# Optimization experiments

Hardware: AMD Instinct MI355X
Metric: run time of the kernel (lower is better)

Reference implementation:

```python
import jax, jax.numpy as jnp
import numpy as np
from jax import lax

WINS = [3, 5, 7, 11, 15, 19]
MAXW = 19
PAD = MAXW // 2 + 1          # 10, matches F.pad(..., max_wh//2+1)
NEG_HALF = (-MAXW) // 2      # -10, matches torch's `-self.max_wh // 2` (floor div)
EPS_IN = 1e-5
EPS_DEV = 1e-6


def _conv(x, w, b, dil):
    # x: [B,C,H,W], w: [O,I,kh,kw], 'same' padding with dilation
    y = lax.conv_general_dilated(x, w, (1, 1), 'SAME',
                                 rhs_dilation=(dil, dil),
                                 dimension_numbers=('NCHW', 'OIHW', 'NCHW'))
    return y + b[None, :, None, None]


def _inorm_relu(y):
    # InstanceNorm2d(affine=False): per-sample per-channel over H,W, biased var
    m = jnp.mean(y, axis=(2, 3), keepdims=True)
    v = jnp.mean((y - m) ** 2, axis=(2, 3), keepdims=True)
    return jax.nn.relu((y - m) * lax.rsqrt(v + EPS_IN))


def _integral(x):
    # x: [B,H,W,C] -> padded double cumsum (integral image) [B,H+2P,W+2P,C]
    xp = jnp.pad(x, ((0, 0), (PAD, PAD), (PAD, PAD), (0, 0)))
    return jnp.cumsum(jnp.cumsum(xp, axis=1), axis=2)


def _box_sum(ii, h, w):
    # 4-corner integral-image lookup; slices reproduce torch offsets exactly
    top = MAXW // 2 - h // 2
    bot = top + h
    left = MAXW // 2 - w // 2
    right = left + w
    top0 = NEG_HALF - h // 2 - 1
    bot0 = top0 + h
    left0 = NEG_HALF - w // 2 - 1
    right0 = left0 + w
    return (ii[:, top:top0, left:left0] + ii[:, bot:bot0, right:right0]
            - ii[:, top:top0, right:right0] - ii[:, bot:bot0, left:left0])


def _multi_window_mean(x):
    # x: [B,H,W,1] -> [B,n_wins,H,W,1] of window means
    ii = _integral(x)
    cnt_ii = _integral(jnp.ones_like(x[:1]))  # [1,...] pixel-count integral
    means = [_box_sum(ii, hw, hw) / _box_sum(cnt_ii, hw, hw) for hw in WINS]
    return jnp.stack(means, axis=1)


def _sauvola(x1, k, R):
    E_x = _multi_window_mean(x1)
    E_x2 = _multi_window_mean(x1 * x1)
    dev = jnp.sqrt(jnp.maximum(E_x2 - E_x ** 2, EPS_DEV))
    return E_x * (1.0 + k * (dev / R - 1.0))  # [B,n,H,W,1]


def setup_inputs() -> dict:
    key = jax.random.key(0)
    ks = jax.random.split(key, 16)
    B, H, W = 4, 768, 768
    base = 4
    chans = [1, 4, 8, 12, 16, 20, 24]
    d = {'x': jax.random.uniform(ks[0], (B, 1, H, W), dtype=jnp.float32)}
    names = ['conv1', 'convs1', 'convs2', 'convs3', 'convs4', 'convs5']
    for i, nm in enumerate(names):
        cin, cout = chans[i], chans[i + 1]
        d[nm + '_w'] = jax.random.normal(ks[1 + i], (cout, cin, 3, 3), dtype=jnp.float32) * 0.1
        d[nm + '_b'] = jax.random.normal(ks[7 + i], (cout,), dtype=jnp.float32) * 0.01
    d['conv2_w'] = jax.random.normal(ks[13], (len(WINS), 24, 3, 3), dtype=jnp.float32) * 0.1
    d['conv2_b'] = jax.random.normal(ks[14], (len(WINS),), dtype=jnp.float32) * 0.01
    d['k'] = jnp.full((1, len(WINS), 1, 1, 1), 0.2, dtype=jnp.float32)
    d['R'] = jnp.full((1, len(WINS), 1, 1, 1), 0.5, dtype=jnp.float32)
    d['alpha'] = jnp.full((1, 1, 1, 1), 16.0, dtype=jnp.float32)
    return d


def reference(x, conv1_w, conv1_b, convs1_w, convs1_b, convs2_w, convs2_b,
              convs3_w, convs3_b, convs4_w, convs4_b, convs5_w, convs5_b,
              conv2_w, conv2_b, k, R, alpha):
    y = _inorm_relu(_conv(x, conv1_w, conv1_b, 1))
    for w, b in ((convs1_w, convs1_b), (convs2_w, convs2_b), (convs3_w, convs3_b),
                 (convs4_w, convs4_b), (convs5_w, convs5_b)):
        y = _inorm_relu(_conv(y, w, b, 2))
    f = jax.nn.softmax(_conv(y, conv2_w, conv2_b, 1), axis=1)  # [B,n,H,W]
    x1 = jnp.transpose(x, (0, 2, 3, 1))                        # [B,H,W,1]
    th = _sauvola(x1, k, R)                                    # [B,n,H,W,1]
    th1 = jnp.sum(f[..., None] * th, axis=1)                   # [B,H,W,1]
    diff = (x1 - th1) * alpha / (1.0 - 0.0)                    # img_range (0,1)
    return jnp.transpose(diff, (0, 3, 1, 2))                   # [B,1,H,W]
```

## Files before the change

### kernel.cpp

```cpp
#include <hip/hip_runtime.h>
#include <math.h>

#define BDIM 256
#define BDIM2 512
typedef __bf16 bf16;
typedef __bf16 bf16x4 __attribute__((ext_vector_type(4)));
typedef __bf16 bf16x8 __attribute__((ext_vector_type(8)));
typedef float f32x4 __attribute__((ext_vector_type(4)));
typedef float f32x2 __attribute__((ext_vector_type(2)));

template <bool V> struct BC { static constexpr bool value = V; };

constexpr int B_ = 4, H_ = 768, W_ = 768;
constexpr int HW_ = H_ * W_;
constexpr int TS = 16;
constexpr int NTB = W_ / TS;
constexpr int NBLK = HW_ / (TS * TS);
constexpr int TS2 = 32;
constexpr int NTB2 = W_ / TS2;
constexpr int NBLK2 = HW_ / (TS2 * TS2);

constexpr int PMAX_FLOATS = 4 * NBLK * 48;
constexpr int OUT_ELEMS   = B_ * HW_;

__device__ void repack_one(const float* __restrict__ src, bf16* __restrict__ dst,
                           int CIN, int CINP, int COUT, int NT16, int KPP)
{
    const int n_ = NT16 * KPP;
    for (int idx = threadIdx.x; idx < n_; idx += BDIM) {
        const int n = idx / KPP, k = idx - n * KPP;
        const int tap = k / CINP, ci = k - tap * CINP;
        float v = 0.f;
        if (n < COUT && tap < 9 && ci < CIN)
            v = src[(n * CIN + ci) * 9 + tap];
        dst[idx] = (bf16)v;
    }
}

__global__ __launch_bounds__(BDIM) void repack_all(
    const float* w0, const float* w1, const float* w2, const float* w3,
    const float* w4, const float* w5, const float* wf,
    bf16* r0, bf16* r1, bf16* r2, bf16* r3, bf16* r4, bf16* r5, bf16* rf)
{
    switch (blockIdx.x) {
        case 0: repack_one(w0, r0, 1,  8,  4,  16, 104); break;
        case 1: repack_one(w1, r1, 4,  8,  8,  16, 104); break;
        case 2: repack_one(w2, r2, 8,  8,  12, 16, 104); break;
        case 3: repack_one(w3, r3, 12, 16, 16, 16, 168); break;
        case 4: repack_one(w4, r4, 16, 16, 20, 32, 168); break;
        case 5: repack_one(w5, r5, 20, 24, 24, 32, 232); break;
        case 6: repack_one(wf, rf, 24, 24, 6,  16, 232); break;
    }
}

template <int CIN, int CINP, int COUT, int DIL, bool FIRST>
__global__ __launch_bounds__(BDIM) void conv_mfma(
    const void* __restrict__ inv,
    const float* __restrict__ prevStats,
    const bf16* __restrict__ wp,
    const float* __restrict__ bias,
    bf16* __restrict__ y,
    float* __restrict__ partials,
    int NBT)
{
    constexpr int TW = TS + 2 * DIL;
    constexpr int KP = ((9 * CINP + 31) / 32) * 32;
    constexpr int KPP = KP + 8;
    constexpr int NT = (COUT + 15) / 16;
    constexpr int KS = KP / 32;
    constexpr int CSTR = (CINP == 16) ? 24 : CINP;
    __shared__ __align__(16) bf16 tile[TW * TW * CSTR];
    __shared__ float sred[4][2 * COUT];

    const int s = blockIdx.x / NBLK;
    const int blk = blockIdx.x - s * NBLK;
    const int ti = blk / NTB, tj = blk - ti * NTB;
    const int i0 = ti * TS - DIL, j0 = tj * TS - DIL;
    const int t = threadIdx.x;
    const bool interior = (i0 >= 0) & (j0 >= 0) &
                          (i0 + TW <= H_) & (j0 + TW <= W_);

    const float* ps = prevStats + s * 2 * CIN;
    auto stage = [&](auto bc) {
        constexpr bool IN = decltype(bc)::value;
        for (int loc = t; loc < TW * TW; loc += BDIM) {
            const int rr = loc / TW, cc = loc - rr * TW;
            const int gi = i0 + rr, gj = j0 + cc;
            bool ok = true;
            if constexpr (!IN)
                ok = (gi >= 0) & (gi < H_) & (gj >= 0) & (gj < W_);
            float lv[CSTR];
#pragma unroll
            for (int c = 0; c < CSTR; ++c) lv[c] = 0.f;
            if (ok) {
                if constexpr (FIRST) {
                    const float* xg = (const float*)inv + (size_t)s * HW_;
                    lv[0] = xg[(size_t)gi * W_ + gj];
                } else {
                    const bf16* ing = (const bf16*)inv +
                                      ((size_t)s * HW_ + (size_t)gi * W_ + gj) * CIN;
                    if constexpr (CIN % 8 == 0) {
#pragma unroll
                        for (int qq = 0; qq < CIN / 8; ++qq) {
                            bf16x8 raw = ((const bf16x8*)ing)[qq];
#pragma unroll
                            for (int u = 0; u < 8; ++u) {
                                const int ci = 8 * qq + u;
                                lv[ci] = fmaxf(fmaf((float)raw[u], ps[2 * ci], ps[2 * ci + 1]), 0.f);
                            }
                        }
                    } else {
#pragma unroll
                        for (int qq = 0; qq < CIN / 4; ++qq) {
                            bf16x4 raw = ((const bf16x4*)ing)[qq];
#pragma unroll
                            for (int u = 0; u < 4; ++u) {
                                const int ci = 4 * qq + u;
                                lv[ci] = fmaxf(fmaf((float)raw[u], ps[2 * ci], ps[2 * ci + 1]), 0.f);
                            }
                        }
                    }
                }
            }
            bf16* lp = tile + loc * CSTR;
#pragma unroll
            for (int g = 0; g < CSTR / 8; ++g) {
                bf16x8 pk;
#pragma unroll
                for (int u = 0; u < 8; ++u) pk[u] = (bf16)lv[8 * g + u];
                *(bf16x8*)(lp + 8 * g) = pk;
            }
        }
    };
    if (interior) stage(BC<true>{}); else stage(BC<false>{});
    __syncthreads();

    const int wave = t >> 6, lane = t & 63, q = lane >> 4, ln = lane & 15;
    f32x4 acc[4][NT];
#pragma unroll
    for (int mt = 0; mt < 4; ++mt)
#pragma unroll
        for (int u = 0; u < NT; ++u) acc[mt][u] = (f32x4){0.f, 0.f, 0.f, 0.f};

    auto aOff = [&](int ks) -> int {
        int k0 = ks * 32 + q * 8;
        int tap = k0 / CINP;
        int ci0 = k0 - tap * CINP;
        if (tap > 8) { tap = 0; ci0 = 0; }
        const int ky = tap / 3, kx = tap - 3 * ky;
        return (ky * DIL * TW + kx * DIL) * CSTR + ci0;
    };

    bf16x8 bfr[NT], bfrN[NT];
    bf16x8 af[4], afN[4];
#pragma unroll
    for (int u = 0; u < NT; ++u)
        bfr[u] = *(const bf16x8*)&wp[(u * 16 + ln) * KPP + q * 8];
    {
        const int ao = aOff(0);
#pragma unroll
        for (int mt = 0; mt < 4; ++mt)
            af[mt] = *(const bf16x8*)&tile[((wave * 4 + mt) * TW + ln) * CSTR + ao];
    }

#pragma unroll
    for (int ks = 0; ks < KS; ++ks) {
        if (ks + 1 < KS) {
#pragma unroll
            for (int u = 0; u < NT; ++u)
                bfrN[u] = *(const bf16x8*)&wp[(u * 16 + ln) * KPP + (ks + 1) * 32 + q * 8];
            const int ao = aOff(ks + 1);
#pragma unroll
            for (int mt = 0; mt < 4; ++mt)
                afN[mt] = *(const bf16x8*)&tile[((wave * 4 + mt) * TW + ln) * CSTR + ao];
        }
#pragma unroll
        for (int mt = 0; mt < 4; ++mt)
#pragma unroll
            for (int u = 0; u < NT; ++u)
                acc[mt][u] = __builtin_amdgcn_mfma_f32_16x16x32_bf16(
                    af[mt], bfr[u], acc[mt][u], 0, 0, 0);
#pragma unroll
        for (int u = 0; u < NT; ++u) bfr[u] = bfrN[u];
#pragma unroll
        for (int mt = 0; mt < 4; ++mt) af[mt] = afN[mt];
    }

#pragma unroll
    for (int u = 0; u < NT; ++u) {
        const int n = u * 16 + ln;
        const float bv = (n < COUT) ? bias[n] : 0.f;
        float s1 = 0.f, s2 = 0.f;
#pragma unroll
        for (int mt = 0; mt < 4; ++mt)
#pragma unroll
            for (int r = 0; r < 4; ++r) {
                const float v = acc[mt][u][r] + bv;
                acc[mt][u][r] = v;
                s1 += v; s2 += v * v;
            }
        s1 += __shfl_xor(s1, 16); s1 += __shfl_xor(s1, 32);
        s2 += __shfl_xor(s2, 16); s2 += __shfl_xor(s2, 32);
        if (lane < 16 && n < COUT) { sred[wave][n] = s1; sred[wave][COUT + n] = s2; }
    }
    __syncthreads();
    if (t < 2 * COUT) {
        partials[(size_t)t * NBT + (size_t)s * NBLK + blk] =
            sred[0][t] + sred[1][t] + sred[2][t] + sred[3][t];
    }

    bf16* ost = tile;
#pragma unroll
    for (int u = 0; u < NT; ++u) {
        const int n = u * 16 + ln;
        if (n < COUT) {
#pragma unroll
            for (int mt = 0; mt < 4; ++mt)
#pragma unroll
                for (int r = 0; r < 4; ++r) {
                    const int pl = (wave * 4 + mt) * 16 + q * 4 + r;
                    ost[pl * COUT + n] = (bf16)acc[mt][u][r];
                }
        }
    }
    __syncthreads();

    const int lr = t >> 4, lc = t & 15;
    bf16* yp = y + (size_t)s * HW_ * COUT +
               ((size_t)(ti * TS + lr) * W_ + (tj * TS + lc)) * COUT;
    const bf16* sp = ost + t * COUT;
    if constexpr (COUT % 8 == 0) {
#pragma unroll
        for (int g = 0; g < COUT / 8; ++g)
            ((bf16x8*)yp)[g] = ((const bf16x8*)sp)[g];
    } else {
#pragma unroll
        for (int g = 0; g < COUT / 4; ++g)
            ((bf16x4*)yp)[g] = ((const bf16x4*)sp)[g];
    }
}

template <int COUT>
__global__ __launch_bounds__(BDIM) void reduce_stats(
    const float* __restrict__ partials, float* __restrict__ stats, int NBT)
{
    const int s = blockIdx.x / COUT;
    const int co = blockIdx.x - s * COUT;
    const float* P1 = partials + (size_t)co * NBT + (size_t)s * NBLK;
    const float* P2 = partials + (size_t)(COUT + co) * NBT + (size_t)s * NBLK;
    float s1 = 0.f, s2 = 0.f;
    for (int k = threadIdx.x; k < NBLK; k += BDIM) {
        s1 += P1[k];
        s2 += P2[k];
    }
#pragma unroll
    for (int off = 32; off; off >>= 1) {
        s1 += __shfl_xor(s1, off);
        s2 += __shfl_xor(s2, off);
    }
    __shared__ float l1[4], l2[4];
    const int lane = threadIdx.x & 63, wave = threadIdx.x >> 6;
    if (lane == 0) { l1[wave] = s1; l2[wave] = s2; }
    __syncthreads();
    if (threadIdx.x == 0) {
        float t1 = l1[0] + l1[1] + l1[2] + l1[3];
        float t2 = l2[0] + l2[1] + l2[2] + l2[3];
        float m = t1 / (float)HW_;
        float var = t2 / (float)HW_ - m * m;
        const float rs = rsqrtf(var + 1e-5f);
        stats[((size_t)s * COUT + co) * 2 + 0] = rs;
        stats[((size_t)s * COUT + co) * 2 + 1] = -m * rs;
    }
}

__global__ __launch_bounds__(BDIM2) void conv2_sauvola(
    const bf16* __restrict__ in, const float* __restrict__ prevStats,
    const bf16* __restrict__ wp, const float* __restrict__ bias,
    const float* __restrict__ x,
    const float* __restrict__ kArr, const float* __restrict__ RArr,
    const float* __restrict__ alphaP, float* __restrict__ outp)
{
    constexpr int CIN = 24, CINP = 24, COUT = 6;
    constexpr int TW = TS2 + 2;
    constexpr int KPP = 232, KS = 7, CSTR = 24;
    constexpr int R9 = 9;
    constexpr int TSW = TS2 + 2 * R9;
    constexpr int ISTR = 51;
    constexpr int SLOG_STR = 7;
    __shared__ __align__(16) bf16 tile[TW * TW * CSTR];
    __shared__ __align__(16) f32x2 I12[(TSW + 1) * ISTR];

    const int s = blockIdx.x / NBLK2;
    const int blk = blockIdx.x - s * NBLK2;
    const int ti = blk / NTB2, tj = blk - ti * NTB2;
    const int i0 = ti * TS2 - 1, j0 = tj * TS2 - 1;
    const int is0 = ti * TS2 - R9, js0 = tj * TS2 - R9;
    const int t = threadIdx.x;
    const float* xs = x + (size_t)s * HW_;
    const bool interior = (is0 >= 0) & (js0 >= 0) &
                          (is0 + TSW <= H_) & (js0 + TSW <= W_);

    const float* ps = prevStats + s * 2 * CIN;
    auto stage = [&](auto bc) {
        constexpr bool IN = decltype(bc)::value;
        for (int loc = t; loc < TW * TW; loc += BDIM2) {
            const int rr = loc / TW, cc = loc - rr * TW;
            const int gi = i0 + rr, gj = j0 + cc;
            bool ok = true;
            if constexpr (!IN)
                ok = (gi >= 0) & (gi < H_) & (gj >= 0) & (gj < W_);
            float lv[CSTR];
#pragma unroll
            for (int c = 0; c < CSTR; ++c) lv[c] = 0.f;
            if (ok) {
                const bf16* ing = in + ((size_t)s * HW_ + (size_t)gi * W_ + gj) * CIN;
#pragma unroll
                for (int qq = 0; qq < CIN / 8; ++qq) {
                    bf16x8 raw = ((const bf16x8*)ing)[qq];
#pragma unroll
                    for (int u = 0; u < 8; ++u) {
                        const int ci = 8 * qq + u;
                        lv[ci] = fmaxf(fmaf((float)raw[u], ps[2 * ci], ps[2 * ci + 1]), 0.f);
                    }
                }
            }
            bf16* lp = tile + loc * CSTR;
#pragma unroll
            for (int g = 0; g < CSTR / 8; ++g) {
                bf16x8 pk;
#pragma unroll
                for (int u = 0; u < 8; ++u) pk[u] = (bf16)lv[8 * g + u];
                *(bf16x8*)(lp + 8 * g) = pk;
            }
        }
        for (int loc = t; loc < TSW * TSW; loc += BDIM2) {
            const int rr = loc / TSW, cc = loc - rr * TSW;
            const int gi = is0 + rr, gj = js0 + cc;
            float v;
            if constexpr (IN) {
                v = xs[(size_t)gi * W_ + gj];
            } else {
                v = 0.f;
                if ((gi >= 0) & (gi < H_) & (gj >= 0) & (gj < W_))
                    v = xs[(size_t)gi * W_ + gj];
            }
            I12[(rr + 1) * ISTR + cc + 1] = (f32x2){v, v * v};
        }
    };
    if (interior) stage(BC<true>{}); else stage(BC<false>{});
    for (int idx = t; idx < (TSW + 1) + TSW; idx += BDIM2) {
        if (idx < TSW + 1) I12[idx] = (f32x2){0.f, 0.f};
        else I12[(idx - (TSW + 1) + 1) * ISTR] = (f32x2){0.f, 0.f};
    }
    __syncthreads();

    const int wave = t >> 6, lane = t & 63, q = lane >> 4, ln = lane & 15;
    f32x4 acc[8];
#pragma unroll
    for (int mt = 0; mt < 8; ++mt) acc[mt] = (f32x4){0.f, 0.f, 0.f, 0.f};

    auto aOff = [&](int ks) -> int {
        int k0 = ks * 32 + q * 8;
        int tap = k0 / CINP;
        int ci0 = k0 - tap * CINP;
        if (tap > 8) { tap = 0; ci0 = 0; }
        const int ky = tap / 3, kx = tap - 3 * ky;
        return (ky * TW + kx) * CSTR + ci0;
    };

#pragma unroll
    for (int ks = 0; ks < KS; ++ks) {
        const bf16x8 bfr = *(const bf16x8*)&wp[ln * KPP + ks * 32 + q * 8];
        const int ao = aOff(ks);
#pragma unroll
        for (int mt = 0; mt < 8; ++mt) {
            const int Mt = wave * 8 + mt;
            const bf16x8 af = *(const bf16x8*)
                &tile[(((Mt >> 1)) * TW + (Mt & 1) * 16 + ln) * CSTR + ao];
            acc[mt] = __builtin_amdgcn_mfma_f32_16x16x32_bf16(af, bfr, acc[mt], 0, 0, 0);
        }
    }
    __syncthreads();

    float* slog = (float*)tile;
    const float bv = (ln < COUT) ? bias[ln] : 0.f;
#pragma unroll
    for (int mt = 0; mt < 8; ++mt)
#pragma unroll
        for (int r = 0; r < 4; ++r)
            if (ln < COUT) {
                const int pl = (wave * 8 + mt) * 16 + q * 4 + r;
                slog[pl * SLOG_STR + ln] = acc[mt][r] + bv;
            }
    if (t < TSW) {
        f32x2* row = I12 + (t + 1) * ISTR;
        f32x2 a = (f32x2){0.f, 0.f};
#pragma unroll 2
        for (int c = 1; c <= TSW; ++c) { a += row[c]; row[c] = a; }
    }
    __syncthreads();

    if (t < TSW) {
        const int c = t + 1;
        f32x2 a = (f32x2){0.f, 0.f};
#pragma unroll 2
        for (int r = 1; r <= TSW; ++r) {
            f32x2* p = &I12[r * ISTR + c];
            a += *p; *p = a;
        }
    }
    float e0[COUT], e1[COUT];
    auto softmax_of = [&](int p, float* e) {
        float mx = slog[p * SLOG_STR];
#pragma unroll
        for (int co = 1; co < COUT; ++co) mx = fmaxf(mx, slog[p * SLOG_STR + co]);
        float sm = 0.f;
#pragma unroll
        for (int co = 0; co < COUT; ++co) { e[co] = __expf(slog[p * SLOG_STR + co] - mx); sm += e[co]; }
        const float inv = 1.f / sm;
#pragma unroll
        for (int co = 0; co < COUT; ++co) e[co] *= inv;
    };
    softmax_of(t, e0);
    softmax_of(t + BDIM2, e1);
    float c0w[6], c1w[6];
#pragma unroll
    for (int wi = 0; wi < 6; ++wi) {
        const float kk = kArr[wi], rr = RArr[wi];
        c0w[wi] = kk / rr;
        c1w[wi] = 1.f - kk;
    }
    const int pr0 = t >> 5, pc0 = t & 31;
    const int pr1 = pr0 + 16, pc1 = pc0;
    const int gi0 = ti * TS2 + pr0, gj0 = tj * TS2 + pc0;
    const int gi1 = ti * TS2 + pr1, gj1 = tj * TS2 + pc1;
    const float xv0 = xs[(size_t)gi0 * W_ + gj0];
    const float xv1 = xs[(size_t)gi1 * W_ + gj1];
    const float alpha = alphaP[0];
    __syncthreads();

    const int wins[6] = {3, 5, 7, 11, 15, 19};
    const float invc_tab[6] = {1.f / 9.f,  1.f / 25.f,  1.f / 49.f,
                               1.f / 121.f, 1.f / 225.f, 1.f / 361.f};
    auto sauv = [&](int pr, int pc, int gi, int gj, const float* e) -> float {
        float th1 = 0.f;
        if (interior) {
#pragma unroll
            for (int wi = 0; wi < 6; ++wi) {
                const int r = wins[wi] >> 1;
                const float invc = invc_tab[wi];
                const int top = pr + R9 - r, bot = pr + R9 + r + 1;
                const int lef = pc + R9 - r, rig = pc + R9 + r + 1;
                const f32x2 Atl = I12[top * ISTR + lef];
                const f32x2 Atr = I12[top * ISTR + rig];
                const f32x2 Abl = I12[bot * ISTR + lef];
                const f32x2 Abr = I12[bot * ISTR + rig];
                const f32x2 sm2 = Abr - Atr - Abl + Atl;
                const float Ex = sm2.x * invc;
                const float Ex2 = sm2.y * invc;
                const float dev = sqrtf(fmaxf(Ex2 - Ex * Ex, 1e-6f));
                const float th = Ex * fmaf(dev, c0w[wi], c1w[wi]);
                th1 = fmaf(e[wi], th, th1);
            }
        } else {
#pragma unroll
            for (int wi = 0; wi < 6; ++wi) {
                const int r = wins[wi] >> 1;
                const int r0 = max(gi - r, 0), r1i = min(gi + r, H_ - 1);
                const int c0 = max(gj - r, 0), c1 = min(gj + r, W_ - 1);
                const float invc = 1.f / (float)((r1i - r0 + 1) * (c1 - c0 + 1));
                const int top = pr + R9 - r, bot = pr + R9 + r + 1;
                const int lef = pc + R9 - r, rig = pc + R9 + r + 1;
                const f32x2 Atl = I12[top * ISTR + lef];
                const f32x2 Atr = I12[top * ISTR + rig];
                const f32x2 Abl = I12[bot * ISTR + lef];
                const f32x2 Abr = I12[bot * ISTR + rig];
                const f32x2 sm2 = Abr - Atr - Abl + Atl;
                const float Ex = sm2.x * invc;
                const float Ex2 = sm2.y * invc;
                const float dev = sqrtf(fmaxf(Ex2 - Ex * Ex, 1e-6f));
                const float th = Ex * fmaf(dev, c0w[wi], c1w[wi]);
                th1 = fmaf(e[wi], th, th1);
            }
        }
        return th1;
    };
    const float th10 = sauv(pr0, pc0, gi0, gj0, e0);
    const float th11 = sauv(pr1, pc1, gi1, gj1, e1);
    outp[(size_t)s * HW_ + (size_t)gi0 * W_ + gj0] = (xv0 - th10) * alpha;
    outp[(size_t)s * HW_ + (size_t)gi1 * W_ + gj1] = (xv1 - th11) * alpha;
}

extern "C" void kernel_launch(void* const* d_in, const int* in_sizes, int n_in,
                              void* d_out, int out_size, void* d_ws, size_t ws_size,
                              hipStream_t stream) {
    const float* x   = (const float*)d_in[0];
    const float* w0  = (const float*)d_in[1];  const float* b0 = (const float*)d_in[2];
    const float* w1  = (const float*)d_in[3];  const float* b1 = (const float*)d_in[4];
    const float* w2  = (const float*)d_in[5];  const float* b2 = (const float*)d_in[6];
    const float* w3  = (const float*)d_in[7];  const float* b3 = (const float*)d_in[8];
    const float* w4  = (const float*)d_in[9];  const float* b4 = (const float*)d_in[10];
    const float* w5  = (const float*)d_in[11]; const float* b5 = (const float*)d_in[12];
    const float* wf  = (const float*)d_in[13]; const float* bf = (const float*)d_in[14];
    const float* kA  = (const float*)d_in[15];
    const float* RA  = (const float*)d_in[16];
    const float* alp = (const float*)d_in[17];
    float* out = (float*)d_out;
    (void)n_in; (void)in_sizes; (void)out_size;

    float* partials = out + (OUT_ELEMS - PMAX_FLOATS - 256);
    float* stats    = out + (OUT_ELEMS - 224);

    auto need = [](int nb) -> size_t {
        size_t o = 0;
        auto al = [&](size_t bytes) { o += (bytes + 255) & ~(size_t)255; };
        al((size_t)nb * HW_ * 20 * 2);
        al((size_t)nb * HW_ * 24 * 2);
        al(1664 * 2); al(1664 * 2); al(1664 * 2); al(2688 * 2);
        al(5376 * 2); al(7424 * 2); al(3712 * 2);
        return o;
    };
    int nb = 1;
    if (ws_size >= need(4)) nb = 4;
    else if (ws_size >= need(2)) nb = 2;

    char* ws = (char*)d_ws;
    size_t off = 0;
    auto alloc = [&](size_t bytes) -> void* {
        void* p = ws + off;
        off += (bytes + 255) & ~(size_t)255;
        return p;
    };
    bf16*  bufA = (bf16*)alloc((size_t)nb * HW_ * 20 * 2);
    bf16*  bufB = (bf16*)alloc((size_t)nb * HW_ * 24 * 2);
    bf16* r0 = (bf16*)alloc(1664 * 2);
    bf16* r1 = (bf16*)alloc(1664 * 2);
    bf16* r2 = (bf16*)alloc(1664 * 2);
    bf16* r3 = (bf16*)alloc(2688 * 2);
    bf16* r4 = (bf16*)alloc(5376 * 2);
    bf16* r5 = (bf16*)alloc(7424 * 2);
    bf16* rf = (bf16*)alloc(3712 * 2);

    const dim3 blk(BDIM);
    const int cg = nb * NBLK;
    const int NBT = nb * NBLK;

    repack_all<<<7, blk, 0, stream>>>(w0, w1, w2, w3, w4, w5, wf,
                                      r0, r1, r2, r3, r4, r5, rf);

    for (int it = 0; it < B_ / nb; ++it) {
        const float* xc   = x   + (size_t)it * nb * HW_;
        float*       outc = out + (size_t)it * nb * HW_;

        conv_mfma<1, 8, 4, 1, true><<<cg, blk, 0, stream>>>(xc, nullptr, r0, b0, bufA, partials, NBT);
        reduce_stats<4><<<nb * 4, blk, 0, stream>>>(partials, stats, NBT);

        conv_mfma<4, 8, 8, 2, false><<<cg, blk, 0, stream>>>(bufA, stats, r1, b1, bufB, partials, NBT);
        reduce_stats<8><<<nb * 8, blk, 0, stream>>>(partials, stats, NBT);

        conv_mfma<8, 8, 12, 2, false><<<cg, blk, 0, stream>>>(bufB, stats, r2, b2, bufA, partials, NBT);
        reduce_stats<12><<<nb * 12, blk, 0, stream>>>(partials, stats, NBT);

        conv_mfma<12, 16, 16, 2, false><<<cg, blk, 0, stream>>>(bufA, stats, r3, b3, bufB, partials, NBT);
        reduce_stats<16><<<nb * 16, blk, 0, stream>>>(partials, stats, NBT);

        conv_mfma<16, 16, 20, 2, false><<<cg, blk, 0, stream>>>(bufB, stats, r4, b4, bufA, partials, NBT);
        reduce_stats<20><<<nb * 20, blk, 0, stream>>>(partials, stats, NBT);

        conv_mfma<20, 24, 24, 2, false><<<cg, blk, 0, stream>>>(bufA, stats, r5, b5, bufB, partials, NBT);
        reduce_stats<24><<<nb * 24, blk, 0, stream>>>(partials, stats, NBT);

        conv2_sauvola<<<nb * NBLK2, dim3(BDIM2), 0, stream>>>(
            bufB, stats, rf, bf, xc, kA, RA, alp, outc);
    }
}
```

Before: 404.6 us.

## Replace per-layer stats reduction kernels with atomics and enlarge conv tiles

```diff
diff --git a/kernel.cpp b/kernel.cpp
--- a/kernel.cpp
+++ b/kernel.cpp
@@ -13,15 +13,13 @@
 
 constexpr int B_ = 4, H_ = 768, W_ = 768;
 constexpr int HW_ = H_ * W_;
-constexpr int TS = 16;
-constexpr int NTB = W_ / TS;
-constexpr int NBLK = HW_ / (TS * TS);
 constexpr int TS2 = 32;
 constexpr int NTB2 = W_ / TS2;
 constexpr int NBLK2 = HW_ / (TS2 * TS2);
 
-constexpr int PMAX_FLOATS = 4 * NBLK * 48;
-constexpr int OUT_ELEMS   = B_ * HW_;
+constexpr int ACC_SLOT_FLOATS = 4 * 48 * 16;
+constexpr int ACC_SLOTS = 24;
+constexpr int ACC_FLOATS = ACC_SLOTS * ACC_SLOT_FLOATS;
 
 __device__ void repack_one(const float* __restrict__ src, bf16* __restrict__ dst,
                            int CIN, int CINP, int COUT, int NT16, int KPP)
@@ -40,7 +38,8 @@
 __global__ __launch_bounds__(BDIM) void repack_all(
     const float* w0, const float* w1, const float* w2, const float* w3,
     const float* w4, const float* w5, const float* wf,
-    bf16* r0, bf16* r1, bf16* r2, bf16* r3, bf16* r4, bf16* r5, bf16* rf)
+    bf16* r0, bf16* r1, bf16* r2, bf16* r3, bf16* r4, bf16* r5, bf16* rf,
+    float* acc)
 {
     switch (blockIdx.x) {
         case 0: repack_one(w0, r0, 1,  8,  4,  16, 104); break;
@@ -50,40 +49,58 @@
         case 4: repack_one(w4, r4, 16, 16, 20, 32, 168); break;
         case 5: repack_one(w5, r5, 20, 24, 24, 32, 232); break;
         case 6: repack_one(wf, rf, 24, 24, 6,  16, 232); break;
+        case 7:
+            for (int idx = threadIdx.x; idx < ACC_FLOATS; idx += BDIM)
+                acc[idx] = 0.f;
+            break;
     }
 }
 
 template <int CIN, int CINP, int COUT, int DIL, bool FIRST>
-__global__ __launch_bounds__(BDIM) void conv_mfma(
+__global__ __launch_bounds__(BDIM2) void conv_mfma(
     const void* __restrict__ inv,
-    const float* __restrict__ prevStats,
+    const float* __restrict__ accPrev,
     const bf16* __restrict__ wp,
     const float* __restrict__ bias,
     bf16* __restrict__ y,
-    float* __restrict__ partials,
-    int NBT)
+    float* __restrict__ accOut)
 {
-    constexpr int TW = TS + 2 * DIL;
+    constexpr int TW = TS2 + 2 * DIL;
     constexpr int KP = ((9 * CINP + 31) / 32) * 32;
     constexpr int KPP = KP + 8;
     constexpr int NT = (COUT + 15) / 16;
     constexpr int KS = KP / 32;
     constexpr int CSTR = (CINP == 16) ? 24 : CINP;
-    __shared__ __align__(16) bf16 tile[TW * TW * CSTR];
-    __shared__ float sred[4][2 * COUT];
-
-    const int s = blockIdx.x / NBLK;
-    const int blk = blockIdx.x - s * NBLK;
-    const int ti = blk / NTB, tj = blk - ti * NTB;
-    const int i0 = ti * TS - DIL, j0 = tj * TS - DIL;
+    constexpr int SMEM = (TW * TW * CSTR > TS2 * TS2 * COUT)
+                             ? TW * TW * CSTR : TS2 * TS2 * COUT;
+    __shared__ __align__(16) bf16 tile[SMEM];
+    __shared__ float sred[8][2 * COUT];
+    __shared__ float psl[2 * CIN];
+
+    const int s = blockIdx.x / NBLK2;
+    const int blk = blockIdx.x - s * NBLK2;
+    const int ti = blk / NTB2, tj = blk - ti * NTB2;
+    const int i0 = ti * TS2 - DIL, j0 = tj * TS2 - DIL;
     const int t = threadIdx.x;
     const bool interior = (i0 >= 0) & (j0 >= 0) &
                           (i0 + TW <= H_) & (j0 + TW <= W_);
 
-    const float* ps = prevStats + s * 2 * CIN;
+    if constexpr (!FIRST) {
+        if (t < CIN) {
+            const float t1 = accPrev[((size_t)s * 48 + t) * 16];
+            const float t2 = accPrev[((size_t)s * 48 + CIN + t) * 16];
+            const float m = t1 / (float)HW_;
+            const float var = t2 / (float)HW_ - m * m;
+            const float rs = rsqrtf(var + 1e-5f);
+            psl[2 * t] = rs;
+            psl[2 * t + 1] = -m * rs;
+        }
+        __syncthreads();
+    }
+
     auto stage = [&](auto bc) {
         constexpr bool IN = decltype(bc)::value;
-        for (int loc = t; loc < TW * TW; loc += BDIM) {
+        for (int loc = t; loc < TW * TW; loc += BDIM2) {
             const int rr = loc / TW, cc = loc - rr * TW;
             const int gi = i0 + rr, gj = j0 + cc;
             bool ok = true;
@@ -106,7 +123,7 @@
 #pragma unroll
                             for (int u = 0; u < 8; ++u) {
                                 const int ci = 8 * qq + u;
-                                lv[ci] = fmaxf(fmaf((float)raw[u], ps[2 * ci], ps[2 * ci + 1]), 0.f);
+                                lv[ci] = fmaxf(fmaf((float)raw[u], psl[2 * ci], psl[2 * ci + 1]), 0.f);
                             }
                         }
                     } else {
@@ -116,7 +133,7 @@
 #pragma unroll
                             for (int u = 0; u < 4; ++u) {
                                 const int ci = 4 * qq + u;
-                                lv[ci] = fmaxf(fmaf((float)raw[u], ps[2 * ci], ps[2 * ci + 1]), 0.f);
+                                lv[ci] = fmaxf(fmaf((float)raw[u], psl[2 * ci], psl[2 * ci + 1]), 0.f);
                             }
                         }
                     }
@@ -136,9 +153,9 @@
     __syncthreads();
 
     const int wave = t >> 6, lane = t & 63, q = lane >> 4, ln = lane & 15;
-    f32x4 acc[4][NT];
-#pragma unroll
-    for (int mt = 0; mt < 4; ++mt)
+    f32x4 acc[8][NT];
+#pragma unroll
+    for (int mt = 0; mt < 8; ++mt)
 #pragma unroll
         for (int u = 0; u < NT; ++u) acc[mt][u] = (f32x4){0.f, 0.f, 0.f, 0.f};
 
@@ -151,39 +168,23 @@
         return (ky * DIL * TW + kx * DIL) * CSTR + ci0;
     };
 
-    bf16x8 bfr[NT], bfrN[NT];
-    bf16x8 af[4], afN[4];
-#pragma unroll
-    for (int u = 0; u < NT; ++u)
-        bfr[u] = *(const bf16x8*)&wp[(u * 16 + ln) * KPP + q * 8];
-    {
-        const int ao = aOff(0);
-#pragma unroll
-        for (int mt = 0; mt < 4; ++mt)
-            af[mt] = *(const bf16x8*)&tile[((wave * 4 + mt) * TW + ln) * CSTR + ao];
-    }
-
 #pragma unroll
     for (int ks = 0; ks < KS; ++ks) {
-        if (ks + 1 < KS) {
-#pragma unroll
-            for (int u = 0; u < NT; ++u)
-                bfrN[u] = *(const bf16x8*)&wp[(u * 16 + ln) * KPP + (ks + 1) * 32 + q * 8];
-            const int ao = aOff(ks + 1);
-#pragma unroll
-            for (int mt = 0; mt < 4; ++mt)
-                afN[mt] = *(const bf16x8*)&tile[((wave * 4 + mt) * TW + ln) * CSTR + ao];
-        }
-#pragma unroll
-        for (int mt = 0; mt < 4; ++mt)
+        bf16x8 bfr[NT];
+#pragma unroll
+        for (int u = 0; u < NT; ++u)
+            bfr[u] = *(const bf16x8*)&wp[(u * 16 + ln) * KPP + ks * 32 + q * 8];
+        const int ao = aOff(ks);
+#pragma unroll
+        for (int mt = 0; mt < 8; ++mt) {
+            const int Mt = wave * 8 + mt;
+            const bf16x8 af = *(const bf16x8*)
+                &tile[(((Mt >> 1)) * TW + (Mt & 1) * 16 + ln) * CSTR + ao];
 #pragma unroll
             for (int u = 0; u < NT; ++u)
                 acc[mt][u] = __builtin_amdgcn_mfma_f32_16x16x32_bf16(
-                    af[mt], bfr[u], acc[mt][u], 0, 0, 0);
-#pragma unroll
-        for (int u = 0; u < NT; ++u) bfr[u] = bfrN[u];
-#pragma unroll
-        for (int mt = 0; mt < 4; ++mt) af[mt] = afN[mt];
+                    af, bfr[u], acc[mt][u], 0, 0, 0);
+        }
     }
 
 #pragma unroll
@@ -192,7 +193,7 @@
         const float bv = (n < COUT) ? bias[n] : 0.f;
         float s1 = 0.f, s2 = 0.f;
 #pragma unroll
-        for (int mt = 0; mt < 4; ++mt)
+        for (int mt = 0; mt < 8; ++mt)
 #pragma unroll
             for (int r = 0; r < 4; ++r) {
                 const float v = acc[mt][u][r] + bv;
@@ -205,8 +206,10 @@
     }
     __syncthreads();
     if (t < 2 * COUT) {
-        partials[(size_t)t * NBT + (size_t)s * NBLK + blk] =
-            sred[0][t] + sred[1][t] + sred[2][t] + sred[3][t];
+        float v = 0.f;
+#pragma unroll
+        for (int w = 0; w < 8; ++w) v += sred[w][t];
+        atomicAdd(&accOut[((size_t)s * 48 + t) * 16], v);
     }
 
     bf16* ost = tile;
@@ -215,66 +218,35 @@
         const int n = u * 16 + ln;
         if (n < COUT) {
 #pragma unroll
-            for (int mt = 0; mt < 4; ++mt)
+            for (int mt = 0; mt < 8; ++mt)
 #pragma unroll
                 for (int r = 0; r < 4; ++r) {
-                    const int pl = (wave * 4 + mt) * 16 + q * 4 + r;
+                    const int pl = (wave * 8 + mt) * 16 + q * 4 + r;
                     ost[pl * COUT + n] = (bf16)acc[mt][u][r];
                 }
         }
     }
     __syncthreads();
 
-    const int lr = t >> 4, lc = t & 15;
-    bf16* yp = y + (size_t)s * HW_ * COUT +
-               ((size_t)(ti * TS + lr) * W_ + (tj * TS + lc)) * COUT;
-    const bf16* sp = ost + t * COUT;
-    if constexpr (COUT % 8 == 0) {
-#pragma unroll
-        for (int g = 0; g < COUT / 8; ++g)
-            ((bf16x8*)yp)[g] = ((const bf16x8*)sp)[g];
-    } else {
-#pragma unroll
-        for (int g = 0; g < COUT / 4; ++g)
-            ((bf16x4*)yp)[g] = ((const bf16x4*)sp)[g];
+    for (int p = t; p < TS2 * TS2; p += BDIM2) {
+        const int lr = p >> 5, lc = p & 31;
+        bf16* yp = y + (size_t)s * HW_ * COUT +
+                   ((size_t)(ti * TS2 + lr) * W_ + (tj * TS2 + lc)) * COUT;
+        const bf16* sp = ost + p * COUT;
+        if constexpr (COUT % 8 == 0) {
+#pragma unroll
+            for (int g = 0; g < COUT / 8; ++g)
+                ((bf16x8*)yp)[g] = ((const bf16x8*)sp)[g];
+        } else {
+#pragma unroll
+            for (int g = 0; g < COUT / 4; ++g)
+                ((bf16x4*)yp)[g] = ((const bf16x4*)sp)[g];
+        }
     }
 }
 
-template <int COUT>
-__global__ __launch_bounds__(BDIM) void reduce_stats(
-    const float* __restrict__ partials, float* __restrict__ stats, int NBT)
-{
-    const int s = blockIdx.x / COUT;
-    const int co = blockIdx.x - s * COUT;
-    const float* P1 = partials + (size_t)co * NBT + (size_t)s * NBLK;
-    const float* P2 = partials + (size_t)(COUT + co) * NBT + (size_t)s * NBLK;
-    float s1 = 0.f, s2 = 0.f;
-    for (int k = threadIdx.x; k < NBLK; k += BDIM) {
-        s1 += P1[k];
-        s2 += P2[k];
-    }
-#pragma unroll
-    for (int off = 32; off; off >>= 1) {
-        s1 += __shfl_xor(s1, off);
-        s2 += __shfl_xor(s2, off);
-    }
-    __shared__ float l1[4], l2[4];
-    const int lane = threadIdx.x & 63, wave = threadIdx.x >> 6;
-    if (lane == 0) { l1[wave] = s1; l2[wave] = s2; }
-    __syncthreads();
-    if (threadIdx.x == 0) {
-        float t1 = l1[0] + l1[1] + l1[2] + l1[3];
-        float t2 = l2[0] + l2[1] + l2[2] + l2[3];
-        float m = t1 / (float)HW_;
-        float var = t2 / (float)HW_ - m * m;
-        const float rs = rsqrtf(var + 1e-5f);
-        stats[((size_t)s * COUT + co) * 2 + 0] = rs;
-        stats[((size_t)s * COUT + co) * 2 + 1] = -m * rs;
-    }
-}
-
 __global__ __launch_bounds__(BDIM2) void conv2_sauvola(
-    const bf16* __restrict__ in, const float* __restrict__ prevStats,
+    const bf16* __restrict__ in, const float* __restrict__ accPrev,
     const bf16* __restrict__ wp, const float* __restrict__ bias,
     const float* __restrict__ x,
     const float* __restrict__ kArr, const float* __restrict__ RArr,
@@ -289,6 +261,7 @@
     constexpr int SLOG_STR = 7;
     __shared__ __align__(16) bf16 tile[TW * TW * CSTR];
     __shared__ __align__(16) f32x2 I12[(TSW + 1) * ISTR];
+    __shared__ float psl[2 * CIN];
 
     const int s = blockIdx.x / NBLK2;
     const int blk = blockIdx.x - s * NBLK2;
@@ -300,7 +273,17 @@
     const bool interior = (is0 >= 0) & (js0 >= 0) &
                           (is0 + TSW <= H_) & (js0 + TSW <= W_);
 
-    const float* ps = prevStats + s * 2 * CIN;
+    if (t < CIN) {
+        const float t1 = accPrev[((size_t)s * 48 + t) * 16];
+        const float t2 = accPrev[((size_t)s * 48 + CIN + t) * 16];
+        const float m = t1 / (float)HW_;
+        const float var = t2 / (float)HW_ - m * m;
+        const float rs = rsqrtf(var + 1e-5f);
+        psl[2 * t] = rs;
+        psl[2 * t + 1] = -m * rs;
+    }
+    __syncthreads();
+
     auto stage = [&](auto bc) {
         constexpr bool IN = decltype(bc)::value;
         for (int loc = t; loc < TW * TW; loc += BDIM2) {
@@ -320,7 +303,7 @@
 #pragma unroll
                     for (int u = 0; u < 8; ++u) {
                         const int ci = 8 * qq + u;
-                        lv[ci] = fmaxf(fmaf((float)raw[u], ps[2 * ci], ps[2 * ci + 1]), 0.f);
+                        lv[ci] = fmaxf(fmaf((float)raw[u], psl[2 * ci], psl[2 * ci + 1]), 0.f);
                     }
                 }
             }
@@ -508,9 +491,6 @@
     float* out = (float*)d_out;
     (void)n_in; (void)in_sizes; (void)out_size;
 
-    float* partials = out + (OUT_ELEMS - PMAX_FLOATS - 256);
-    float* stats    = out + (OUT_ELEMS - 224);
-
     auto need = [](int nb) -> size_t {
         size_t o = 0;
         auto al = [&](size_t bytes) { o += (bytes + 255) & ~(size_t)255; };
@@ -518,6 +498,7 @@
         al((size_t)nb * HW_ * 24 * 2);
         al(1664 * 2); al(1664 * 2); al(1664 * 2); al(2688 * 2);
         al(5376 * 2); al(7424 * 2); al(3712 * 2);
+        al((size_t)ACC_FLOATS * 4);
         return o;
     };
     int nb = 1;
@@ -540,37 +521,32 @@
     bf16* r4 = (bf16*)alloc(5376 * 2);
     bf16* r5 = (bf16*)alloc(7424 * 2);
     bf16* rf = (bf16*)alloc(3712 * 2);
-
-    const dim3 blk(BDIM);
-    const int cg = nb * NBLK;
-    const int NBT = nb * NBLK;
-
-    repack_all<<<7, blk, 0, stream>>>(w0, w1, w2, w3, w4, w5, wf,
-                                      r0, r1, r2, r3, r4, r5, rf);
+    float* acc = (float*)alloc((size_t)ACC_FLOATS * 4);
+
+    const int cg = nb * NBLK2;
+
+    repack_all<<<8, dim3(BDIM), 0, stream>>>(w0, w1, w2, w3, w4, w5, wf,
+                                             r0, r1, r2, r3, r4, r5, rf, acc);
 
     for (int it = 0; it < B_ / nb; ++it) {
         const float* xc   = x   + (size_t)it * nb * HW_;
         float*       outc = out + (size_t)it * nb * HW_;
-
-        conv_mfma<1, 8, 4, 1, true><<<cg, blk, 0, stream>>>(xc, nullptr, r0, b0, bufA, partials, NBT);
-        reduce_stats<4><<<nb * 4, blk, 0, stream>>>(partials, stats, NBT);
-
-        conv_mfma<4, 8, 8, 2, false><<<cg, blk, 0, stream>>>(bufA, stats, r1, b1, bufB, partials, NBT);
-        reduce_stats<8><<<nb * 8, blk, 0, stream>>>(partials, stats, NBT);
-
-        conv_mfma<8, 8, 12, 2, false><<<cg, blk, 0, stream>>>(bufB, stats, r2, b2, bufA, partials, NBT);
-        reduce_stats<12><<<nb * 12, blk, 0, stream>>>(partials, stats, NBT);
-
-        conv_mfma<12, 16, 16, 2, false><<<cg, blk, 0, stream>>>(bufA, stats, r3, b3, bufB, partials, NBT);
-        reduce_stats<16><<<nb * 16, blk, 0, stream>>>(partials, stats, NBT);
-
-        conv_mfma<16, 16, 20, 2, false><<<cg, blk, 0, stream>>>(bufB, stats, r4, b4, bufA, partials, NBT);
-        reduce_stats<20><<<nb * 20, blk, 0, stream>>>(partials, stats, NBT);
-
-        conv_mfma<20, 24, 24, 2, false><<<cg, blk, 0, stream>>>(bufA, stats, r5, b5, bufB, partials, NBT);
-        reduce_stats<24><<<nb * 24, blk, 0, stream>>>(partials, stats, NBT);
-
-        conv2_sauvola<<<nb * NBLK2, dim3(BDIM2), 0, stream>>>(
-            bufB, stats, rf, bf, xc, kA, RA, alp, outc);
+        float* sl = acc + (size_t)it * 6 * ACC_SLOT_FLOATS;
+
+        conv_mfma<1, 8, 4, 1, true><<<cg, dim3(BDIM2), 0, stream>>>(
+            xc, nullptr, r0, b0, bufA, sl + 0 * ACC_SLOT_FLOATS);
+        conv_mfma<4, 8, 8, 2, false><<<cg, dim3(BDIM2), 0, stream>>>(
+            bufA, sl + 0 * ACC_SLOT_FLOATS, r1, b1, bufB, sl + 1 * ACC_SLOT_FLOATS);
+        conv_mfma<8, 8, 12, 2, false><<<cg, dim3(BDIM2), 0, stream>>>(
+            bufB, sl + 1 * ACC_SLOT_FLOATS, r2, b2, bufA, sl + 2 * ACC_SLOT_FLOATS);
+        conv_mfma<12, 16, 16, 2, false><<<cg, dim3(BDIM2), 0, stream>>>(
+            bufA, sl + 2 * ACC_SLOT_FLOATS, r3, b3, bufB, sl + 3 * ACC_SLOT_FLOATS);
+        conv_mfma<16, 16, 20, 2, false><<<cg, dim3(BDIM2), 0, stream>>>(
+            bufB, sl + 3 * ACC_SLOT_FLOATS, r4, b4, bufA, sl + 4 * ACC_SLOT_FLOATS);
+        conv_mfma<20, 24, 24, 2, false><<<cg, dim3(BDIM2), 0, stream>>>(
+            bufA, sl + 4 * ACC_SLOT_FLOATS, r5, b5, bufB, sl + 5 * ACC_SLOT_FLOATS);
+
+        conv2_sauvola<<<cg, dim3(BDIM2), 0, stream>>>(
+            bufB, sl + 5 * ACC_SLOT_FLOATS, rf, bf, xc, kA, RA, alp, outc);
     }
 }
```

Result: slower. 525.1 us (+29.8%).
